# Performance work log

Measured on AMD Instinct MI355X. Metric: run time of the kernel, lower is better.

## Reference

```python
import jax, jax.numpy as jnp
import numpy as np

B, H, N, D = 4, 16, 4096, 64
M = 266  # nb_features = int(D * ln(D))
KERNEL_EPS = 1e-4


def _gaussian_orthogonal_random_matrix(nb_rows, nb_cols, rng):
    # Faithful to gaussian_orthogonal_random_matrix with scaling=0.
    blocks = []
    for _ in range(nb_rows // nb_cols):
        q, _ = np.linalg.qr(rng.standard_normal((nb_cols, nb_cols)))
        blocks.append(q.T)
    rem = nb_rows - (nb_rows // nb_cols) * nb_cols
    if rem > 0:
        q, _ = np.linalg.qr(rng.standard_normal((nb_cols, nb_cols)))
        blocks.append(q.T[:rem])
    final = np.concatenate(blocks, axis=0)
    mult = np.linalg.norm(rng.standard_normal((nb_rows, nb_cols)), axis=1)
    return (mult[:, None] * final).astype(np.float32)


def setup_inputs() -> dict:
    key = jax.random.key(0)
    kq, kk, kv = jax.random.split(key, 3)
    q = jax.random.normal(kq, (B, H, N, D), dtype=jnp.float32)
    k = jax.random.normal(kk, (B, H, N, D), dtype=jnp.float32)
    v = jax.random.normal(kv, (B, H, N, D), dtype=jnp.float32)
    proj = jnp.asarray(_gaussian_orthogonal_random_matrix(M, D, np.random.default_rng(0)))
    return {"q": q, "k": k, "v": v, "projection_matrix": proj}


def _softmax_kernel(x, proj, is_query):
    d = x.shape[-1]
    data_normalizer = d ** (-0.25)
    ratio = proj.shape[0] ** (-0.5)
    # [b,h,n,m]
    data_dash = jnp.einsum("bhnd,md->bhnm", data_normalizer * x, proj)
    diag = jnp.sum(x * x, axis=-1, keepdims=True) * 0.5 * (data_normalizer ** 2)
    if is_query:
        mx = jax.lax.stop_gradient(jnp.max(data_dash, axis=-1, keepdims=True))
    else:
        mx = jax.lax.stop_gradient(jnp.max(data_dash, axis=(-1, -2), keepdims=True))
    return ratio * (jnp.exp(data_dash - diag - mx) + KERNEL_EPS)


def _linear_attention(q, k, v):
    k_cumsum = jnp.sum(k, axis=-2)                       # [b,h,m]
    D_ = jnp.einsum("bhnm,bhm->bhn", q, k_cumsum)
    D_inv = 1.0 / jnp.where(D_ == 0, 1e-5, D_)
    context = jnp.einsum("bhnm,bhne->bhme", k, v)        # [b,h,m,e]
    return jnp.einsum("bhme,bhnm,bhn->bhne", context, q, D_inv)


def reference(q, k, v, projection_matrix):
    qp = _softmax_kernel(q, projection_matrix, is_query=True)
    kp = _softmax_kernel(k, projection_matrix, is_query=False)
    return _linear_attention(qp, kp, v)
```

## Files before the change

### kernel.cpp

```cpp
#include <hip/hip_runtime.h>
#include <math.h>


#define BH 64
#define NTOK 4096
#define DIM 64
#define MF 266
#define MPAD 272
#define NCH 4
#define CHROWS 1024
#define SUBS 16
#define RATIO 0.06131393394849658f
#define DNORM 0.35355339059327373f
#define DIAGC 0.0625f
#define L2E   1.4426950408889634f
#define KEPS 1e-4f

#define PSTR 72
#define QSTR 296

typedef _Float16 half8 __attribute__((ext_vector_type(8)));
typedef _Float16 half4 __attribute__((ext_vector_type(4)));
typedef __fp16 fp16x2 __attribute__((ext_vector_type(2)));
typedef float floatx4 __attribute__((ext_vector_type(4)));
typedef short short8 __attribute__((ext_vector_type(8)));
typedef short short4s __attribute__((ext_vector_type(4)));

__device__ __forceinline__ short f2h_bits(float f) {
    union { _Float16 h; short s; } u; u.h = (_Float16)f; return u.s;
}
__device__ __forceinline__ float h2f(short s) {
    union { short s; _Float16 h; } u; u.s = s; return (float)u.h;
}
__device__ __forceinline__ unsigned cvt_pk_bf16(float lo, float hi) {
    unsigned r;
    asm("v_cvt_pk_bf16_f32 %0, %1, %2" : "=v"(r) : "v"(lo), "v"(hi));
    return r;
}
__device__ __forceinline__ float fexp2(float x) {
    float r;
    asm("v_exp_f32 %0, %1" : "=v"(r) : "v"(x));
    return r;
}
__device__ __forceinline__ unsigned encf(float f) {
    unsigned u = __float_as_uint(f);
    return (u & 0x80000000u) ? ~u : (u | 0x80000000u);
}
__device__ __forceinline__ float decf(unsigned u) {
    u = (u & 0x80000000u) ? (u & 0x7FFFFFFFu) : ~u;
    return __uint_as_float(u);
}

__global__ __launch_bounds__(512, 4)
void k_pass(const float* __restrict__ kin, const float* __restrict__ vin,
            const float* __restrict__ proj, float* __restrict__ A0p,
            float* __restrict__ S0p, unsigned int* __restrict__ gmax)
{
    __shared__ __align__(16) short kL[2][64 * PSTR];
    __shared__ __align__(16) short vT[2][64 * PSTR];
    __shared__ float diagL[2][64];
    __shared__ __align__(16) short epS[16][16 * PSTR];

    const int tid = threadIdx.x;
    const int l = tid & 63, w = tid >> 6;
    const int c = tid & 15, g = (tid >> 4) & 3;
    const int h    = blockIdx.x >> 8;
    const int rest = blockIdx.x & 255;
    const int bh   = rest >> 2;
    const int ch   = rest & 3;
    const int nT = (h == 1 && w == 0) ? 2 : 1;
    const int t0 = (h == 0) ? w : (8 + w);

    const float PSC = DNORM * L2E;
    half8 pj0[2], pj1[2];
    #pragma unroll
    for (int it = 0; it < 2; ++it) {
        half8 z;
        #pragma unroll
        for (int j = 0; j < 8; ++j) z[j] = (_Float16)0.f;
        pj0[it] = z; pj1[it] = z;
        const int t = it ? 16 : t0;
        const int f = 16 * t + c;
        if (it < nT && f < MF) {
            const float* ps = proj + (size_t)f * 64 + 8 * g;
            float4 x0 = *(const float4*)ps;
            float4 x1 = *(const float4*)(ps + 4);
            float4 x2 = *(const float4*)(ps + 32);
            float4 x3 = *(const float4*)(ps + 36);
            half8 b0, b1;
            b0[0]=(_Float16)(PSC*x0.x); b0[1]=(_Float16)(PSC*x0.y);
            b0[2]=(_Float16)(PSC*x0.z); b0[3]=(_Float16)(PSC*x0.w);
            b0[4]=(_Float16)(PSC*x1.x); b0[5]=(_Float16)(PSC*x1.y);
            b0[6]=(_Float16)(PSC*x1.z); b0[7]=(_Float16)(PSC*x1.w);
            b1[0]=(_Float16)(PSC*x2.x); b1[1]=(_Float16)(PSC*x2.y);
            b1[2]=(_Float16)(PSC*x2.z); b1[3]=(_Float16)(PSC*x2.w);
            b1[4]=(_Float16)(PSC*x3.x); b1[5]=(_Float16)(PSC*x3.y);
            b1[6]=(_Float16)(PSC*x3.z); b1[7]=(_Float16)(PSC*x3.w);
            pj0[it] = b0; pj1[it] = b1;
        }
    }

    const float* kb = kin + ((size_t)bh * NTOK + (size_t)ch * CHROWS) * DIM;
    const float* vb = vin + ((size_t)bh * NTOK + (size_t)ch * CHROWS) * DIM;

    const int srow = 8 * w + (l >> 3);
    const int sd0  = (l & 7) * 8;
    const int vrow = l;
    const int ve0  = 8 * w;

    floatx4 acc[2][4];
    #pragma unroll
    for (int it = 0; it < 2; ++it)
        #pragma unroll
        for (int et = 0; et < 4; ++et) {
            acc[it][et][0]=0.f; acc[it][et][1]=0.f; acc[it][et][2]=0.f; acc[it][et][3]=0.f;
        }
    float s0acc[2] = {0.f, 0.f};
    float dmax = -3.0e38f;

    float4 ka0, ka1, va0, va1;

    auto issue_loads = [&](int s) {
        const float* ks = kb + (size_t)(64 * s + srow) * DIM + sd0;
        ka0 = *(const float4*)ks;
        ka1 = *(const float4*)(ks + 4);
        const float* vs = vb + (size_t)(64 * s + vrow) * DIM + ve0;
        va0 = *(const float4*)vs;
        va1 = *(const float4*)(vs + 4);
    };

    auto stage_write = [&](int buf) {
        union { fp16x2 h2[4]; short8 s8; } uk;
        uk.h2[0] = __builtin_amdgcn_cvt_pkrtz(ka0.x, ka0.y);
        uk.h2[1] = __builtin_amdgcn_cvt_pkrtz(ka0.z, ka0.w);
        uk.h2[2] = __builtin_amdgcn_cvt_pkrtz(ka1.x, ka1.y);
        uk.h2[3] = __builtin_amdgcn_cvt_pkrtz(ka1.z, ka1.w);
        *(short8*)&kL[buf][srow * PSTR + sd0] = uk.s8;
        float ds2 = ka0.x*ka0.x + ka0.y*ka0.y + ka0.z*ka0.z + ka0.w*ka0.w
                  + ka1.x*ka1.x + ka1.y*ka1.y + ka1.z*ka1.z + ka1.w*ka1.w;
        ds2 += __shfl_xor(ds2, 1);
        ds2 += __shfl_xor(ds2, 2);
        ds2 += __shfl_xor(ds2, 4);
        if ((l & 7) == 0) diagL[buf][srow] = ds2 * (DIAGC * L2E);
        unsigned pv0 = cvt_pk_bf16(va0.x, va0.y);
        unsigned pv1 = cvt_pk_bf16(va0.z, va0.w);
        unsigned pv2 = cvt_pk_bf16(va1.x, va1.y);
        unsigned pv3 = cvt_pk_bf16(va1.z, va1.w);
        vT[buf][(ve0 + 0) * PSTR + vrow] = (short)(pv0 & 0xFFFF);
        vT[buf][(ve0 + 1) * PSTR + vrow] = (short)(pv0 >> 16);
        vT[buf][(ve0 + 2) * PSTR + vrow] = (short)(pv1 & 0xFFFF);
        vT[buf][(ve0 + 3) * PSTR + vrow] = (short)(pv1 >> 16);
        vT[buf][(ve0 + 4) * PSTR + vrow] = (short)(pv2 & 0xFFFF);
        vT[buf][(ve0 + 5) * PSTR + vrow] = (short)(pv2 >> 16);
        vT[buf][(ve0 + 6) * PSTR + vrow] = (short)(pv3 & 0xFFFF);
        vT[buf][(ve0 + 7) * PSTR + vrow] = (short)(pv3 >> 16);
    };

    issue_loads(0);
    stage_write(0);
    __syncthreads();

    for (int s = 0; s < SUBS; ++s) {
        const int cur = s & 1;
        const bool more = (s + 1 < SUBS);
        if (more) issue_loads(s + 1);

        #pragma unroll
        for (int nt = 0; nt < 4; ++nt) {
            const half8 a0 = *(const half8*)&kL[cur][(16 * nt + c) * PSTR + 8 * g];
            const half8 a1 = *(const half8*)&kL[cur][(16 * nt + c) * PSTR + 8 * g + 32];
            const float4 dg4 = *(const float4*)&diagL[cur][16 * nt + 4 * g];
            const float dgr[4] = {dg4.x, dg4.y, dg4.z, dg4.w};
            #pragma unroll
            for (int it = 0; it < 2; ++it) {
                if (it < nT) {
                    floatx4 d = {0.f, 0.f, 0.f, 0.f};
                    d = __builtin_amdgcn_mfma_f32_16x16x32_f16(a0, pj0[it], d, 0, 0, 0);
                    d = __builtin_amdgcn_mfma_f32_16x16x32_f16(a1, pj1[it], d, 0, 0, 0);
                    const bool t16 = (it == 1);
                    float ev[4];
                    #pragma unroll
                    for (int r = 0; r < 4; ++r) {
                        const float ddv = d[r];
                        if (!t16 || c < 10) dmax = fmaxf(dmax, ddv);
                        float e = fexp2(ddv - dgr[r]);
                        if (t16 && c == 15) e = 1.0f;
                        s0acc[it] += e;
                        ev[r] = e;
                    }
                    uint2 pk;
                    pk.x = cvt_pk_bf16(ev[0], ev[1]);
                    pk.y = cvt_pk_bf16(ev[2], ev[3]);
                    *(uint2*)&epS[2 * w + it][c * PSTR + 16 * nt + 4 * g] = pk;
                }
            }
        }

        #pragma unroll
        for (int ntp = 0; ntp < 2; ++ntp) {
            const short8 bq0 = *(const short8*)&epS[2 * w][c * PSTR + 32 * ntp + 8 * g];
            short8 bq1;
            if (nT == 2) bq1 = *(const short8*)&epS[2 * w + 1][c * PSTR + 32 * ntp + 8 * g];
            #pragma unroll
            for (int et = 0; et < 4; ++et) {
                const short8 av = *(const short8*)&vT[cur][(16 * et + c) * PSTR + 32 * ntp + 8 * g];
                acc[0][et] = __builtin_amdgcn_mfma_f32_16x16x32_bf16(av, bq0, acc[0][et], 0, 0, 0);
                if (nT == 2)
                    acc[1][et] = __builtin_amdgcn_mfma_f32_16x16x32_bf16(av, bq1, acc[1][et], 0, 0, 0);
            }
        }

        if (more) {
            stage_write(cur ^ 1);
            __syncthreads();
        }
    }

    {
        float* dst = A0p + (size_t)(bh * NCH + ch) * (MPAD * 64);
        #pragma unroll
        for (int it = 0; it < 2; ++it) {
            if (it < nT) {
                const int t = it ? 16 : t0;
                #pragma unroll
                for (int et = 0; et < 4; ++et)
                    *(floatx4*)&dst[(size_t)(16 * t + c) * 64 + 16 * et + 4 * g] = acc[it][et];
            }
        }
    }
    #pragma unroll
    for (int it = 0; it < 2; ++it) {
        if (it < nT) {
            const int t = it ? 16 : t0;
            float s = s0acc[it];
            s += __shfl_xor(s, 16);
            s += __shfl_xor(s, 32);
            if (g == 0 && (t < 16 || c < 10))
                atomicAdd(&S0p[bh * MPAD + 16 * t + c], s);
        }
    }
    #pragma unroll
    for (int sft = 1; sft <= 32; sft <<= 1) dmax = fmaxf(dmax, __shfl_xor(dmax, sft));
    if (l == 0) atomicMax(gmax + bh, encf(dmax));
}

__global__ __launch_bounds__(512, 1)
void reduce_ctx(const float* __restrict__ A0p, const float* __restrict__ S0p,
                const unsigned int* __restrict__ gmax, const float* __restrict__ proj,
                short* __restrict__ ctxw, short* __restrict__ projw)
{
    __shared__ __align__(16) short L[65 * 288];
    const int bh = blockIdx.x, tid = threadIdx.x;
    if (bh < 17) {
        #pragma unroll
        for (int rep = 0; rep < 2; ++rep) {
            const int idx = rep * 512 + tid;
            const int f = 16 * bh + (idx >> 6);
            const int d = idx & 63;
            const float val = (f < MF) ? proj[(size_t)f * 64 + d] * (DNORM * L2E) : 0.f;
            projw[(size_t)f * 64 + d] = f2h_bits(val);
        }
    }
    const float emx = fexp2(-decf(gmax[bh]));
    const int e = tid & 63, mi = tid >> 6;
    const float* base = A0p + (size_t)bh * NCH * MPAD * 64;
    float vs = 0.f;
    #pragma unroll
    for (int c2 = 0; c2 < NCH; ++c2)
        vs += base[(size_t)c2 * MPAD * 64 + (size_t)271 * 64 + e];
    const float vsr = vs * KEPS;
    for (int m = mi; m < 288; m += 8) {
        float val = 0.f;
        if (m < MF) {
            float s = 0.f;
            #pragma unroll
            for (int c2 = 0; c2 < NCH; ++c2)
                s += base[(size_t)c2 * MPAD * 64 + (size_t)m * 64 + e];
            val = RATIO * (emx * s + vsr);
        }
        L[e * 288 + m] = f2h_bits(val);
    }
    for (int m = tid; m < 288; m += 512) {
        float val = 0.f;
        if (m < MF) val = RATIO * (emx * S0p[bh * MPAD + m] + KEPS * 4096.0f);
        L[64 * 288 + m] = f2h_bits(val);
    }
    __syncthreads();
    short* dst = ctxw + (size_t)bh * (65 * 288);
    for (int idx = tid; idx < 65 * 36; idx += 512)
        *(short8*)(dst + idx * 8) = *(const short8*)&L[idx * 8];
}

__global__ __launch_bounds__(512, 2)
void q_pass(const float* __restrict__ qin, const short* __restrict__ projw,
            const short* __restrict__ ctxw, float* __restrict__ outp)
{
    __shared__ __align__(16) short projL[MPAD * PSTR];
    __shared__ __align__(16) short ctxL[65 * QSTR];

    const int tid = threadIdx.x;
    const int bh = blockIdx.x >> 5, rt = blockIdx.x & 31;
    const int c = tid & 15, g = (tid >> 4) & 3, w = tid >> 6;

    for (int idx = tid; idx < MPAD * 8; idx += 512) {
        const int r = idx >> 3, s = idx & 7;
        *(short8*)&projL[r * PSTR + s * 8] = *(const short8*)(projw + (size_t)r * 64 + s * 8);
    }
    {
        const short* src = ctxw + (size_t)bh * (65 * 288);
        for (int idx = tid; idx < 65 * 36; idx += 512) {
            const int r = idx / 36, s = idx - r * 36;
            *(short8*)&ctxL[r * QSTR + s * 8] = *(const short8*)(src + r * 288 + s * 8);
        }
    }
    half8 bf0, bf1;
    float dsum = 0.f;
    {
        const float* qs = qin + ((size_t)bh * NTOK + rt * 128 + 16 * w + c) * DIM;
        #pragma unroll
        for (int ksi = 0; ksi < 2; ++ksi) {
            const float* p4 = qs + ksi * 32 + 8 * g;
            float4 x0 = *(const float4*)p4;
            float4 x1 = *(const float4*)(p4 + 4);
            dsum += x0.x*x0.x + x0.y*x0.y + x0.z*x0.z + x0.w*x0.w
                  + x1.x*x1.x + x1.y*x1.y + x1.z*x1.z + x1.w*x1.w;
            half8& bf = ksi ? bf1 : bf0;
            bf[0]=(_Float16)x0.x; bf[1]=(_Float16)x0.y; bf[2]=(_Float16)x0.z; bf[3]=(_Float16)x0.w;
            bf[4]=(_Float16)x1.x; bf[5]=(_Float16)x1.y; bf[6]=(_Float16)x1.z; bf[7]=(_Float16)x1.w;
        }
    }
    float t1 = dsum + __shfl_xor(dsum, 16);
    const float diagc = (t1 + __shfl_xor(t1, 32)) * (DIAGC * L2E);

    __syncthreads();

    floatx4 dd[17];
    #pragma unroll
    for (int t = 0; t < 17; ++t) {
        const short* ap = &projL[(16 * t + c) * PSTR + 8 * g];
        half8 a0 = *(const half8*)ap;
        half8 a1 = *(const half8*)(ap + 32);
        floatx4 d = {0.f, 0.f, 0.f, 0.f};
        d = __builtin_amdgcn_mfma_f32_16x16x32_f16(a0, bf0, d, 0, 0, 0);
        d = __builtin_amdgcn_mfma_f32_16x16x32_f16(a1, bf1, d, 0, 0, 0);
        dd[t] = d;
    }
    float mx = -3.0e38f;
    #pragma unroll
    for (int t = 0; t < 17; ++t) {
        #pragma unroll
        for (int r2 = 0; r2 < 4; ++r2) {
            const bool fval = (t < 16) || (4 * g + r2 < 10);
            if (fval) mx = fmaxf(mx, dd[t][r2]);
        }
    }
    mx = fmaxf(mx, __shfl_xor(mx, 16));
    mx = fmaxf(mx, __shfl_xor(mx, 32));

    half4 bq[17];
    float denp = 0.f;
    const float sh = diagc + mx;
    #pragma unroll
    for (int t = 0; t < 17; ++t) {
        half4 b;
        #pragma unroll
        for (int r2 = 0; r2 < 4; ++r2) {
            float val = fexp2(dd[t][r2] - sh) + KEPS;
            b[r2] = (_Float16)val;
            denp += val * h2f(ctxL[64 * QSTR + 16 * t + 4 * g + r2]);
        }
        bq[t] = b;
    }
    denp += __shfl_xor(denp, 16);
    denp += __shfl_xor(denp, 32);

    floatx4 acc[4];
    #pragma unroll
    for (int i = 0; i < 4; ++i) { acc[i][0]=0.f; acc[i][1]=0.f; acc[i][2]=0.f; acc[i][3]=0.f; }
    #pragma unroll
    for (int e4 = 0; e4 < 4; ++e4) {
        #pragma unroll
        for (int t = 0; t < 17; ++t) {
            half4 a4 = *(const half4*)&ctxL[(16 * e4 + c) * QSTR + 16 * t + 4 * g];
            acc[e4] = __builtin_amdgcn_mfma_f32_16x16x16f16(a4, bq[t], acc[e4], 0, 0, 0);
        }
    }
    float den = (denp == 0.f) ? 1e-5f : denp;
    const float inv = 1.0f / den;
    float* ob = outp + ((size_t)bh * NTOK + rt * 128 + 16 * w + c) * DIM;
    #pragma unroll
    for (int e4 = 0; e4 < 4; ++e4) {
        float4 o = make_float4(acc[e4][0] * inv, acc[e4][1] * inv,
                               acc[e4][2] * inv, acc[e4][3] * inv);
        *(float4*)(ob + 16 * e4 + 4 * g) = o;
    }
}

extern "C" void kernel_launch(void* const* d_in, const int* in_sizes, int n_in,
                              void* d_out, int out_size, void* d_ws, size_t ws_size,
                              hipStream_t stream)
{
    const float* q    = (const float*)d_in[0];
    const float* k    = (const float*)d_in[1];
    const float* v    = (const float*)d_in[2];
    const float* proj = (const float*)d_in[3];
    float* out = (float*)d_out;
    float* ws  = (float*)d_ws;

    const size_t offS = (size_t)BH * NCH * MPAD * 64;
    const size_t offG = offS + (size_t)BH * MPAD;
    const size_t offC = offG + 64;
    const size_t offP = offC + (size_t)BH * 65 * 288 / 2;

    float* A0p = ws;
    float* S0p = ws + offS;
    unsigned int* gmax = (unsigned int*)(ws + offG);
    short* ctxw = (short*)(ws + offC);
    short* projw = (short*)(ws + offP);

    (void)hipMemsetAsync(S0p, 0, ((size_t)BH * MPAD + 64) * sizeof(float), stream);
    hipLaunchKernelGGL(k_pass, dim3(BH * NCH * 2), dim3(512), 0, stream,
                       k, v, proj, A0p, S0p, gmax);
    hipLaunchKernelGGL(reduce_ctx, dim3(BH), dim3(512), 0, stream,
                       A0p, S0p, gmax, proj, ctxw, projw);
    hipLaunchKernelGGL(q_pass, dim3(BH * 32), dim3(512), 0, stream,
                       q, projw, ctxw, out);
}
```

Measured before the change: 139.7 us.

## Split reduce_ctx across four blocks per head and double q_pass rows per block

reduce_ctx now launches four blocks per batch-head, each reducing a 16-column slice of the context, so 256 blocks run instead of 64 and the small reduction kernel fills more CUs. q_pass processes 256 rows per block in two 128-row iterations, so the projection matrix and context are staged into shared memory once per 256 rows and redundant staging traffic halves. In exchange q_pass has half as many blocks (1024), which lowers parallelism and serialises two row groups within each block.

Result: faster. 133.0 us (-4.8%).

```diff
diff --git a/kernel.cpp b/kernel.cpp
--- a/kernel.cpp
+++ b/kernel.cpp
@@ -244,14 +244,15 @@
     if (l == 0) atomicMax(gmax + bh, encf(dmax));
 }
 
-__global__ __launch_bounds__(512, 1)
+__global__ __launch_bounds__(512, 2)
 void reduce_ctx(const float* __restrict__ A0p, const float* __restrict__ S0p,
                 const unsigned int* __restrict__ gmax, const float* __restrict__ proj,
                 short* __restrict__ ctxw, short* __restrict__ projw)
 {
-    __shared__ __align__(16) short L[65 * 288];
-    const int bh = blockIdx.x, tid = threadIdx.x;
-    if (bh < 17) {
+    __shared__ __align__(16) short L[17 * 288];
+    const int bh = blockIdx.x >> 2, q = blockIdx.x & 3;
+    const int tid = threadIdx.x;
+    if (q == 0 && bh < 17) {
         #pragma unroll
         for (int rep = 0; rep < 2; ++rep) {
             const int idx = rep * 512 + tid;
@@ -262,14 +263,16 @@
         }
     }
     const float emx = fexp2(-decf(gmax[bh]));
-    const int e = tid & 63, mi = tid >> 6;
+    const int el = tid & 15;
+    const int e  = 16 * q + el;
+    const int mi = tid >> 4;
     const float* base = A0p + (size_t)bh * NCH * MPAD * 64;
     float vs = 0.f;
     #pragma unroll
     for (int c2 = 0; c2 < NCH; ++c2)
         vs += base[(size_t)c2 * MPAD * 64 + (size_t)271 * 64 + e];
     const float vsr = vs * KEPS;
-    for (int m = mi; m < 288; m += 8) {
+    for (int m = mi; m < 288; m += 32) {
         float val = 0.f;
         if (m < MF) {
             float s = 0.f;
@@ -278,17 +281,24 @@
                 s += base[(size_t)c2 * MPAD * 64 + (size_t)m * 64 + e];
             val = RATIO * (emx * s + vsr);
         }
-        L[e * 288 + m] = f2h_bits(val);
-    }
-    for (int m = tid; m < 288; m += 512) {
-        float val = 0.f;
-        if (m < MF) val = RATIO * (emx * S0p[bh * MPAD + m] + KEPS * 4096.0f);
-        L[64 * 288 + m] = f2h_bits(val);
+        L[el * 288 + m] = f2h_bits(val);
+    }
+    if (q == 0) {
+        for (int m = tid; m < 288; m += 512) {
+            float val = 0.f;
+            if (m < MF) val = RATIO * (emx * S0p[bh * MPAD + m] + KEPS * 4096.0f);
+            L[16 * 288 + m] = f2h_bits(val);
+        }
     }
     __syncthreads();
-    short* dst = ctxw + (size_t)bh * (65 * 288);
-    for (int idx = tid; idx < 65 * 36; idx += 512)
+    short* dst = ctxw + (size_t)bh * (65 * 288) + (size_t)q * (16 * 288);
+    for (int idx = tid; idx < 16 * 36; idx += 512)
         *(short8*)(dst + idx * 8) = *(const short8*)&L[idx * 8];
+    if (q == 0) {
+        short* kdst = ctxw + (size_t)bh * (65 * 288) + (size_t)64 * 288;
+        if (tid < 36)
+            *(short8*)(kdst + tid * 8) = *(const short8*)&L[16 * 288 + tid * 8];
+    }
 }
 
 __global__ __launch_bounds__(512, 2)
@@ -299,7 +309,7 @@
     __shared__ __align__(16) short ctxL[65 * QSTR];
 
     const int tid = threadIdx.x;
-    const int bh = blockIdx.x >> 5, rt = blockIdx.x & 31;
+    const int bh = blockIdx.x >> 4, rt = blockIdx.x & 15;
     const int c = tid & 15, g = (tid >> 4) & 3, w = tid >> 6;
 
     for (int idx = tid; idx < MPAD * 8; idx += 512) {
@@ -313,86 +323,90 @@
             *(short8*)&ctxL[r * QSTR + s * 8] = *(const short8*)(src + r * 288 + s * 8);
         }
     }
-    half8 bf0, bf1;
-    float dsum = 0.f;
-    {
-        const float* qs = qin + ((size_t)bh * NTOK + rt * 128 + 16 * w + c) * DIM;
-        #pragma unroll
-        for (int ksi = 0; ksi < 2; ++ksi) {
-            const float* p4 = qs + ksi * 32 + 8 * g;
-            float4 x0 = *(const float4*)p4;
-            float4 x1 = *(const float4*)(p4 + 4);
-            dsum += x0.x*x0.x + x0.y*x0.y + x0.z*x0.z + x0.w*x0.w
-                  + x1.x*x1.x + x1.y*x1.y + x1.z*x1.z + x1.w*x1.w;
-            half8& bf = ksi ? bf1 : bf0;
-            bf[0]=(_Float16)x0.x; bf[1]=(_Float16)x0.y; bf[2]=(_Float16)x0.z; bf[3]=(_Float16)x0.w;
-            bf[4]=(_Float16)x1.x; bf[5]=(_Float16)x1.y; bf[6]=(_Float16)x1.z; bf[7]=(_Float16)x1.w;
-        }
-    }
-    float t1 = dsum + __shfl_xor(dsum, 16);
-    const float diagc = (t1 + __shfl_xor(t1, 32)) * (DIAGC * L2E);
-
     __syncthreads();
 
-    floatx4 dd[17];
-    #pragma unroll
-    for (int t = 0; t < 17; ++t) {
-        const short* ap = &projL[(16 * t + c) * PSTR + 8 * g];
-        half8 a0 = *(const half8*)ap;
-        half8 a1 = *(const half8*)(ap + 32);
-        floatx4 d = {0.f, 0.f, 0.f, 0.f};
-        d = __builtin_amdgcn_mfma_f32_16x16x32_f16(a0, bf0, d, 0, 0, 0);
-        d = __builtin_amdgcn_mfma_f32_16x16x32_f16(a1, bf1, d, 0, 0, 0);
-        dd[t] = d;
-    }
-    float mx = -3.0e38f;
-    #pragma unroll
-    for (int t = 0; t < 17; ++t) {
-        #pragma unroll
-        for (int r2 = 0; r2 < 4; ++r2) {
-            const bool fval = (t < 16) || (4 * g + r2 < 10);
-            if (fval) mx = fmaxf(mx, dd[t][r2]);
-        }
-    }
-    mx = fmaxf(mx, __shfl_xor(mx, 16));
-    mx = fmaxf(mx, __shfl_xor(mx, 32));
-
-    half4 bq[17];
-    float denp = 0.f;
-    const float sh = diagc + mx;
-    #pragma unroll
-    for (int t = 0; t < 17; ++t) {
-        half4 b;
-        #pragma unroll
-        for (int r2 = 0; r2 < 4; ++r2) {
-            float val = fexp2(dd[t][r2] - sh) + KEPS;
-            b[r2] = (_Float16)val;
-            denp += val * h2f(ctxL[64 * QSTR + 16 * t + 4 * g + r2]);
-        }
-        bq[t] = b;
-    }
-    denp += __shfl_xor(denp, 16);
-    denp += __shfl_xor(denp, 32);
-
-    floatx4 acc[4];
-    #pragma unroll
-    for (int i = 0; i < 4; ++i) { acc[i][0]=0.f; acc[i][1]=0.f; acc[i][2]=0.f; acc[i][3]=0.f; }
-    #pragma unroll
-    for (int e4 = 0; e4 < 4; ++e4) {
+    #pragma unroll 1
+    for (int rg = 0; rg < 2; ++rg) {
+        const int rowbase = rt * 256 + rg * 128;
+        half8 bf0, bf1;
+        float dsum = 0.f;
+        {
+            const float* qs = qin + ((size_t)bh * NTOK + rowbase + 16 * w + c) * DIM;
+            #pragma unroll
+            for (int ksi = 0; ksi < 2; ++ksi) {
+                const float* p4 = qs + ksi * 32 + 8 * g;
+                float4 x0 = *(const float4*)p4;
+                float4 x1 = *(const float4*)(p4 + 4);
+                dsum += x0.x*x0.x + x0.y*x0.y + x0.z*x0.z + x0.w*x0.w
+                      + x1.x*x1.x + x1.y*x1.y + x1.z*x1.z + x1.w*x1.w;
+                half8& bf = ksi ? bf1 : bf0;
+                bf[0]=(_Float16)x0.x; bf[1]=(_Float16)x0.y; bf[2]=(_Float16)x0.z; bf[3]=(_Float16)x0.w;
+                bf[4]=(_Float16)x1.x; bf[5]=(_Float16)x1.y; bf[6]=(_Float16)x1.z; bf[7]=(_Float16)x1.w;
+            }
+        }
+        float t1 = dsum + __shfl_xor(dsum, 16);
+        const float diagc = (t1 + __shfl_xor(t1, 32)) * (DIAGC * L2E);
+
+        floatx4 dd[17];
         #pragma unroll
         for (int t = 0; t < 17; ++t) {
-            half4 a4 = *(const half4*)&ctxL[(16 * e4 + c) * QSTR + 16 * t + 4 * g];
-            acc[e4] = __builtin_amdgcn_mfma_f32_16x16x16f16(a4, bq[t], acc[e4], 0, 0, 0);
-        }
-    }
-    float den = (denp == 0.f) ? 1e-5f : denp;
-    const float inv = 1.0f / den;
-    float* ob = outp + ((size_t)bh * NTOK + rt * 128 + 16 * w + c) * DIM;
-    #pragma unroll
-    for (int e4 = 0; e4 < 4; ++e4) {
-        float4 o = make_float4(acc[e4][0] * inv, acc[e4][1] * inv,
-                               acc[e4][2] * inv, acc[e4][3] * inv);
-        *(float4*)(ob + 16 * e4 + 4 * g) = o;
+            const short* ap = &projL[(16 * t + c) * PSTR + 8 * g];
+            half8 a0 = *(const half8*)ap;
+            half8 a1 = *(const half8*)(ap + 32);
+            floatx4 d = {0.f, 0.f, 0.f, 0.f};
+            d = __builtin_amdgcn_mfma_f32_16x16x32_f16(a0, bf0, d, 0, 0, 0);
+            d = __builtin_amdgcn_mfma_f32_16x16x32_f16(a1, bf1, d, 0, 0, 0);
+            dd[t] = d;
+        }
+        float mx = -3.0e38f;
+        #pragma unroll
+        for (int t = 0; t < 17; ++t) {
+            #pragma unroll
+            for (int r2 = 0; r2 < 4; ++r2) {
+                const bool fval = (t < 16) || (4 * g + r2 < 10);
+                if (fval) mx = fmaxf(mx, dd[t][r2]);
+            }
+        }
+        mx = fmaxf(mx, __shfl_xor(mx, 16));
+        mx = fmaxf(mx, __shfl_xor(mx, 32));
+
+        half4 bq[17];
+        float denp = 0.f;
+        const float sh = diagc + mx;
+        #pragma unroll
+        for (int t = 0; t < 17; ++t) {
+            half4 b;
+            #pragma unroll
+            for (int r2 = 0; r2 < 4; ++r2) {
+                float val = fexp2(dd[t][r2] - sh) + KEPS;
+                b[r2] = (_Float16)val;
+                denp += val * h2f(ctxL[64 * QSTR + 16 * t + 4 * g + r2]);
+            }
+            bq[t] = b;
+        }
+        denp += __shfl_xor(denp, 16);
+        denp += __shfl_xor(denp, 32);
+
+        floatx4 acc[4];
+        #pragma unroll
+        for (int i = 0; i < 4; ++i) { acc[i][0]=0.f; acc[i][1]=0.f; acc[i][2]=0.f; acc[i][3]=0.f; }
+        #pragma unroll
+        for (int e4 = 0; e4 < 4; ++e4) {
+            #pragma unroll
+            for (int t = 0; t < 17; ++t) {
+                half4 a4 = *(const half4*)&ctxL[(16 * e4 + c) * QSTR + 16 * t + 4 * g];
+                acc[e4] = __builtin_amdgcn_mfma_f32_16x16x16f16(a4, bq[t], acc[e4], 0, 0, 0);
+            }
+        }
+        float den = (denp == 0.f) ? 1e-5f : denp;
+        const float inv = 1.0f / den;
+        float* ob = outp + ((size_t)bh * NTOK + rowbase + 16 * w + c) * DIM;
+        #pragma unroll
+        for (int e4 = 0; e4 < 4; ++e4) {
+            float4 o = make_float4(acc[e4][0] * inv, acc[e4][1] * inv,
+                                   acc[e4][2] * inv, acc[e4][3] * inv);
+            *(float4*)(ob + 16 * e4 + 4 * g) = o;
+        }
     }
 }
 
@@ -421,8 +435,8 @@
     (void)hipMemsetAsync(S0p, 0, ((size_t)BH * MPAD + 64) * sizeof(float), stream);
     hipLaunchKernelGGL(k_pass, dim3(BH * NCH * 2), dim3(512), 0, stream,
                        k, v, proj, A0p, S0p, gmax);
-    hipLaunchKernelGGL(reduce_ctx, dim3(BH), dim3(512), 0, stream,
+    hipLaunchKernelGGL(reduce_ctx, dim3(BH * 4), dim3(512), 0, stream,
                        A0p, S0p, gmax, proj, ctxw, projw);
-    hipLaunchKernelGGL(q_pass, dim3(BH * 32), dim3(512), 0, stream,
+    hipLaunchKernelGGL(q_pass, dim3(BH * 16), dim3(512), 0, stream,
                        q, projw, ctxw, out);
 }
```
